# Kernel optimization log

Measured on AMD Instinct MI355X. Metric: run time of the kernel, lower is better.

The kernel has to match this reference:

```python
import jax, jax.numpy as jnp
import numpy as np

D_MODEL = 512
HEAD_NUM = 8
EPS = 1e-5


def setup_inputs() -> dict:
    key = jax.random.key(0)
    ks = jax.random.split(key, 7)
    B, S, D = 2, 4096, D_MODEL
    scale = 1.0 / np.sqrt(D)
    return {
        "x": jax.random.normal(ks[0], (B, S, D), dtype=jnp.float32),
        "Wq": jax.random.normal(ks[1], (D, D), dtype=jnp.float32) * scale,
        "bq": jnp.zeros((D,), dtype=jnp.float32),
        "Wk": jax.random.normal(ks[2], (D, D), dtype=jnp.float32) * scale,
        "bk": jnp.zeros((D,), dtype=jnp.float32),
        "Wv": jax.random.normal(ks[3], (D, D), dtype=jnp.float32) * scale,
        "bv": jnp.zeros((D,), dtype=jnp.float32),
        "gamma": jnp.ones((D,), dtype=jnp.float32),
        "beta": jnp.zeros((D,), dtype=jnp.float32),
    }


def reference(x, Wq, bq, Wk, bk, Wv, bv, gamma, beta):
    B, S, D = x.shape
    H = HEAD_NUM
    hd = D // H  # q_k_head_dim == v_head_dim == 64
    q = (x @ Wq + bq).reshape(B, H, S, hd)  # faithful to torch .view (no transpose)
    k = (x @ Wk + bk).reshape(B, H, S, hd)
    v = (x @ Wv + bv).reshape(B, H, S, hd)
    # [B,H,S,S] score matrix, materialized exactly as the original does
    scores = jnp.einsum("bhqd,bhkd->bhqk", q, k) / jnp.sqrt(jnp.float32(hd))
    attn_w = jax.nn.softmax(scores, axis=-1)
    attn = jnp.einsum("bhqk,bhkd->bhqd", attn_w, v).reshape(B, S, D)
    h = x + attn
    mu = jnp.mean(h, axis=-1, keepdims=True)
    var = jnp.var(h, axis=-1, keepdims=True)
    y = (h - mu) / jnp.sqrt(var + EPS) * gamma + beta
    return y
```

## Files before the change

### kernel.cpp

```cpp
#include <hip/hip_runtime.h>
#include <stdint.h>

#define D_ 512
#define S_ 4096
#define HD 64
#define CHUNK (S_*HD)

typedef short short8 __attribute__((ext_vector_type(8)));
typedef unsigned short ushort8 __attribute__((ext_vector_type(8)));
typedef float f32x16 __attribute__((ext_vector_type(16)));
typedef float f32x4 __attribute__((ext_vector_type(4)));

__device__ __forceinline__ float b2f(unsigned short u){
  unsigned x = ((unsigned)u) << 16;
  return __builtin_bit_cast(float, x);
}
__device__ __forceinline__ unsigned short f2b(float f){
  unsigned x = __builtin_bit_cast(unsigned, f);
  return (unsigned short)((x + 0x7fffu + ((x >> 16) & 1u)) >> 16);
}
__device__ __forceinline__ unsigned cvt_pk_bf16(float lo, float hi){
  unsigned r; asm("v_cvt_pk_bf16_f32 %0, %1, %2" : "=v"(r) : "v"(lo), "v"(hi)); return r;
}
__device__ __forceinline__ float fexp2(float x){
  float r; asm("v_exp_f32 %0, %1" : "=v"(r) : "v"(x)); return r;
}
__device__ __forceinline__ void gload16(const void* g, void* l){
  __builtin_amdgcn_global_load_lds((__attribute__((address_space(1))) void*)g,
                                   (__attribute__((address_space(3))) void*)l, 16, 0, 0);
}

__global__ void k_convert(const float* __restrict__ x, unsigned short* __restrict__ xb,
                          const float* __restrict__ Wq, const float* __restrict__ Wk,
                          const float* __restrict__ Wv, unsigned short* __restrict__ wt){
  __shared__ __align__(16) float t[32][33];
  if (blockIdx.x < 2048){
    int i = blockIdx.x * blockDim.x + threadIdx.x;
    const float4* xv = (const float4*)x;
    float4 a = xv[i*2], b = xv[i*2+1];
    ushort8 o;
    o[0]=f2b(a.x); o[1]=f2b(a.y); o[2]=f2b(a.z); o[3]=f2b(a.w);
    o[4]=f2b(b.x); o[5]=f2b(b.y); o[6]=f2b(b.z); o[7]=f2b(b.w);
    ((ushort8*)xb)[i] = o;
    return;
  }
  const int i = blockIdx.x - 2048;
  const int z = i >> 8, rem = i & 255;
  const int k0 = (rem & 15) * 32, n0 = (rem >> 4) * 32;
  const float* W = (z==0) ? Wq : ((z==1) ? Wk : Wv);
  unsigned short* o = wt + z * D_ * D_;
  int r = threadIdx.x >> 3, c4 = (threadIdx.x & 7) * 4;
  float4 vv = *(const float4*)&W[(k0+r)*D_ + n0 + c4];
  t[r][c4+0]=vv.x; t[r][c4+1]=vv.y; t[r][c4+2]=vv.z; t[r][c4+3]=vv.w;
  __syncthreads();
  unsigned short* dst = &o[(n0+r)*D_ + k0 + c4];
  dst[0]=f2b(t[c4+0][r]); dst[1]=f2b(t[c4+1][r]);
  dst[2]=f2b(t[c4+2][r]); dst[3]=f2b(t[c4+3][r]);
}

__global__ void __launch_bounds__(256) k_gemm(const unsigned short* __restrict__ xb,
                                              const unsigned short* __restrict__ wt,
                                              const float* __restrict__ bq,
                                              const float* __restrict__ bk,
                                              const float* __restrict__ bv,
                                              unsigned short* __restrict__ q,
                                              unsigned short* __restrict__ k,
                                              unsigned short* __restrict__ v){
  __shared__ __align__(16) unsigned short At[2][128*32];
  __shared__ __align__(16) unsigned short Bt[2][128*32];
  const int mat = blockIdx.z;
  const unsigned short* w = wt + mat * D_ * D_;
  const float* bias = (mat==0) ? bq : ((mat==1) ? bk : bv);
  unsigned short* out = (mat==0) ? q : ((mat==1) ? k : v);
  const int m0 = blockIdx.x * 128, n0 = blockIdx.y * 128;
  const int tid = threadIdx.x, lane = tid & 63, wv = tid >> 6;
  const int wm = wv >> 1, wn = wv & 1;
  const int l15 = lane & 15, l4 = lane >> 4;

  f32x4 acc[4][4] = {};

  auto stage = [&](int kt, int sel){
    const int kbase = kt * 32;
    #pragma unroll
    for (int j = 0; j < 2; j++){
      const int loff = wv*2048 + j*1024 + lane*16;
      const int row = loff >> 6;
      const int c = (loff >> 4) & 3;
      gload16(xb + (m0+row)*D_ + kbase + ((c ^ (row&3)) << 3),
              (char*)At[sel] + wv*2048 + j*1024);
      gload16(w  + (n0+row)*D_ + kbase + ((c ^ (row&3)) << 3),
              (char*)Bt[sel] + wv*2048 + j*1024);
    }
  };

  stage(0, 0);
  int buf = 0;
  for (int kt = 0; kt < 16; ++kt){
    __syncthreads();
    if (kt + 1 < 16) stage(kt + 1, buf ^ 1);
    short8 af[4], bf[4];
    #pragma unroll
    for (int mf = 0; mf < 4; mf++){
      const int row = wm*64 + mf*16 + l15;
      af[mf] = *(const short8*)((const char*)At[buf] + row*64 + ((l4*16) ^ ((row&3)<<4)));
    }
    #pragma unroll
    for (int nf = 0; nf < 4; nf++){
      const int row = wn*64 + nf*16 + l15;
      bf[nf] = *(const short8*)((const char*)Bt[buf] + row*64 + ((l4*16) ^ ((row&3)<<4)));
    }
    #pragma unroll
    for (int mf = 0; mf < 4; mf++)
      #pragma unroll
      for (int nf = 0; nf < 4; nf++)
        acc[mf][nf] = __builtin_amdgcn_mfma_f32_16x16x32_bf16(af[mf], bf[nf], acc[mf][nf], 0,0,0);
    buf ^= 1;
  }
  #pragma unroll
  for (int nf = 0; nf < 4; nf++){
    const int n = n0 + wn*64 + nf*16 + l15;
    const float bval = bias[n];
    #pragma unroll
    for (int mf = 0; mf < 4; mf++){
      #pragma unroll
      for (int r = 0; r < 4; r++){
        const int m = m0 + wm*64 + mf*16 + l4*4 + r;
        out[m*D_ + n] = f2b(acc[mf][nf][r] + bval);
      }
    }
  }
}

__global__ void k_transpose_v(const unsigned short* __restrict__ v, unsigned short* __restrict__ vt){
  __shared__ __align__(16) unsigned short t[64][72];
  const int bh = blockIdx.y, s0 = blockIdx.x * 64;
  const unsigned short* vc = v + bh * CHUNK;
  unsigned short* vtc = vt + bh * CHUNK;
  const int tid = threadIdx.x;
  #pragma unroll
  for (int j = 0; j < 2; j++){
    const int e = j*2048 + tid*8;
    const int row = e >> 6, col = e & 63;
    *(ushort8*)&t[row][col] = *(const ushort8*)&vc[(s0+row)*HD + col];
  }
  __syncthreads();
  const int d = tid >> 2, sc0 = (tid & 3) * 16;
  ushort8 o0, o1;
  #pragma unroll
  for (int j = 0; j < 4; j++){
    o0[j]   = t[sc0 + j     ][d];
    o0[j+4] = t[sc0 + 8 + j ][d];
    o1[j]   = t[sc0 + 4 + j ][d];
    o1[j+4] = t[sc0 + 12 + j][d];
  }
  *(ushort8*)&vtc[d*S_ + s0 + sc0]     = o0;
  *(ushort8*)&vtc[d*S_ + s0 + sc0 + 8] = o1;
}

__global__ void __launch_bounds__(256, 4) k_attn_part(const unsigned short* __restrict__ q,
                                                      const unsigned short* __restrict__ k,
                                                      const unsigned short* __restrict__ vt,
                                                      unsigned short* __restrict__ Op0,
                                                      unsigned short* __restrict__ Op1,
                                                      float2* __restrict__ ml0,
                                                      float2* __restrict__ ml1){
  __shared__ __align__(16) char smem[32768];
  const int bid = blockIdx.x;
  const int c8 = bid & 7, j = bid >> 3;
  const int bh   = 2*c8 + (j & 1);
  const int qblk = (j >> 1) & 31;
  const int half = (j >> 6) & 1;

  const int tid = threadIdx.x, lane = tid & 63, wv = tid >> 6;
  const int l31 = lane & 31, hi = lane >> 5;
  const unsigned short* qc  = q  + bh * CHUNK;
  const unsigned short* kc  = k  + bh * CHUNK;
  const unsigned short* vtc = vt + bh * CHUNK;
  unsigned short* Op = half ? Op1 : Op0;
  float2* ml = half ? ml1 : ml0;
  const int q0 = qblk * 128 + wv * 32;
  const int kvbase = half * 2048;

  short8 qf[4];
  {
    const int row = q0 + l31;
    #pragma unroll
    for (int kb = 0; kb < 4; kb++){
      ushort8 raw = *(const ushort8*)(qc + row*HD + kb*16 + hi*8);
      union { ushort8 u; short8 s; } cc;
      #pragma unroll
      for (int jj = 0; jj < 8; jj++) cc.u[jj] = f2b(b2f(raw[jj]) * (0.125f * 1.44269504f));
      qf[kb] = cc.s;
    }
  }

  f32x16 o0 = {}; f32x16 o1 = {};
  float lrun = 0.f;

  auto stage = [&](int t, int sel){
    const int kv0 = kvbase + t * 64;
    char* kb_ = smem + sel*8192 + wv*2048;
    char* vb_ = smem + 16384 + sel*8192 + wv*2048;
    #pragma unroll
    for (int jj = 0; jj < 2; jj++){
      const int loff = wv*2048 + jj*1024 + lane*16;
      const int row = loff >> 7;
      const int c = (loff >> 4) & 7;
      gload16(kc  + (kv0+row)*HD + ((c ^ (row&7)) << 3), kb_ + jj*1024);
      gload16(vtc + row*S_ + kv0 + ((c ^ (row&7)) << 3), vb_ + jj*1024);
    }
  };

  stage(0, 0);
  int buf = 0;
  const int NT = 2048 / 64;
  for (int t = 0; t < NT; ++t){
    __syncthreads();
    if (t + 1 < NT) stage(t + 1, buf ^ 1);
    const char* kbuf = smem + buf*8192;
    const char* vbuf = smem + 16384 + buf*8192;

    f32x16 st0 = {}; f32x16 st1 = {};
    const int xr = (l31 & 7) << 4;
    #pragma unroll
    for (int kb = 0; kb < 4; kb++){
      const int off = kb*32 + hi*16;
      short8 kf0 = *(const short8*)(kbuf + l31*128        + (off ^ xr));
      short8 kf1 = *(const short8*)(kbuf + (32+l31)*128   + (off ^ xr));
      st0 = __builtin_amdgcn_mfma_f32_32x32x16_bf16(kf0, qf[kb], st0, 0,0,0);
      st1 = __builtin_amdgcn_mfma_f32_32x32x16_bf16(kf1, qf[kb], st1, 0,0,0);
    }

    float s0a = 0.f, s1a = 0.f, s2a = 0.f, s3a = 0.f;
    #pragma unroll
    for (int r = 0; r < 8; r++){
      st0[r]   = fexp2(st0[r]);   s0a += st0[r];
      st0[r+8] = fexp2(st0[r+8]); s1a += st0[r+8];
      st1[r]   = fexp2(st1[r]);   s2a += st1[r];
      st1[r+8] = fexp2(st1[r+8]); s3a += st1[r+8];
    }
    float sum = (s0a + s1a) + (s2a + s3a);
    sum += __shfl_xor(sum, 32);
    lrun += sum;

    short8 pf[4];
    #pragma unroll
    for (int kb = 0; kb < 4; kb++){
      const f32x16& s = (kb < 2) ? st0 : st1;
      const int rb = (kb & 1) * 8;
      union { unsigned u[4]; short8 s8; } pu;
      pu.u[0] = cvt_pk_bf16(s[rb+0], s[rb+1]);
      pu.u[1] = cvt_pk_bf16(s[rb+2], s[rb+3]);
      pu.u[2] = cvt_pk_bf16(s[rb+4], s[rb+5]);
      pu.u[3] = cvt_pk_bf16(s[rb+6], s[rb+7]);
      pf[kb] = pu.s8;
    }

    #pragma unroll
    for (int kb = 0; kb < 4; kb++){
      const int off = kb*32 + hi*16;
      short8 vf0 = *(const short8*)(vbuf + l31*128      + (off ^ xr));
      short8 vf1 = *(const short8*)(vbuf + (32+l31)*128 + (off ^ xr));
      o0 = __builtin_amdgcn_mfma_f32_32x32x16_bf16(vf0, pf[kb], o0, 0,0,0);
      o1 = __builtin_amdgcn_mfma_f32_32x32x16_bf16(vf1, pf[kb], o1, 0,0,0);
    }
    buf ^= 1;
  }

  __syncthreads();
  {
    float* po = (float*)(void*)smem + wv*2048;
    #pragma unroll
    for (int r = 0; r < 16; r++){
      const int d = (r&3) + 8*(r>>2) + 4*hi;
      po[l31*64 + d]      = o0[r];
      po[l31*64 + 32 + d] = o1[r];
    }
  }
  if (hi == 0){
    ml[bh*S_ + q0 + l31] = make_float2(0.0f, lrun);
  }
  __syncthreads();
  {
    const int rr = lane >> 1, hf = lane & 1;
    const float* prow = (const float*)(void*)smem + wv*2048 + rr*64 + hf*32;
    unsigned short* dst = Op + (bh*S_ + q0 + rr)*HD + hf*32;
    #pragma unroll
    for (int blk = 0; blk < 4; blk++){
      ushort8 w8;
      #pragma unroll
      for (int jj = 0; jj < 8; jj++) w8[jj] = f2b(prow[blk*8 + jj]);
      *(ushort8*)(dst + blk*8) = w8;
    }
  }
}

__global__ void k_merge_ln(const unsigned short* __restrict__ Op0,
                           const unsigned short* __restrict__ Op1,
                           const float2* __restrict__ ml0,
                           const float2* __restrict__ ml1,
                           const float* __restrict__ x,
                           const float* __restrict__ gamma,
                           const float* __restrict__ beta,
                           float* __restrict__ out){
  const int row = blockIdx.x * 4 + (threadIdx.x >> 6);
  const int lane = threadIdx.x & 63;
  const int bh = row >> 9;
  const int s_attn = ((row & 511) << 3) + (lane >> 3);
  const int d0 = (lane & 7) * 8;
  const int oidx = (bh*S_ + s_attn)*HD + d0;
  ushort8 u0 = *(const ushort8*)(Op0 + oidx);
  ushort8 u1 = *(const ushort8*)(Op1 + oidx);
  const float2 a = ml0[bh*S_ + s_attn];
  const float2 c = ml1[bh*S_ + s_attn];
  const float M  = fmaxf(a.x, c.x);
  const float e1 = exp2f(a.x - M), e2 = exp2f(c.x - M);
  const float inv = 1.0f / (e1*a.y + e2*c.y);
  const float w1 = e1 * inv, w2 = e2 * inv;

  const float* xr = x + row*D_ + lane*8;
  float4 a0 = *(const float4*)xr, a1 = *(const float4*)(xr + 4);
  float h[8];
  h[0]=a0.x; h[1]=a0.y; h[2]=a0.z; h[3]=a0.w; h[4]=a1.x; h[5]=a1.y; h[6]=a1.z; h[7]=a1.w;
  #pragma unroll
  for (int jj = 0; jj < 8; jj++) h[jj] += w1*b2f(u0[jj]) + w2*b2f(u1[jj]);

  float sm = 0.f, ss = 0.f;
  #pragma unroll
  for (int jj = 0; jj < 8; jj++){ sm += h[jj]; ss += h[jj]*h[jj]; }
  #pragma unroll
  for (int msk = 1; msk < 64; msk <<= 1){ sm += __shfl_xor(sm, msk); ss += __shfl_xor(ss, msk); }
  const float mu = sm * (1.f/512.f);
  const float var = ss * (1.f/512.f) - mu*mu;
  const float rs = rsqrtf(var + 1e-5f);
  const float* g = gamma + lane*8;
  const float* be = beta + lane*8;
  float4 w0, w3;
  w0.x = (h[0]-mu)*rs*g[0] + be[0];
  w0.y = (h[1]-mu)*rs*g[1] + be[1];
  w0.z = (h[2]-mu)*rs*g[2] + be[2];
  w0.w = (h[3]-mu)*rs*g[3] + be[3];
  w3.x = (h[4]-mu)*rs*g[4] + be[4];
  w3.y = (h[5]-mu)*rs*g[5] + be[5];
  w3.z = (h[6]-mu)*rs*g[6] + be[6];
  w3.w = (h[7]-mu)*rs*g[7] + be[7];
  float* op = out + row*D_ + lane*8;
  *(float4*)op = w0;
  *(float4*)(op + 4) = w3;
}

extern "C" void kernel_launch(void* const* d_in, const int* in_sizes, int n_in,
                              void* d_out, int out_size, void* d_ws, size_t ws_size,
                              hipStream_t stream){
  const float* x     = (const float*)d_in[0];
  const float* Wq    = (const float*)d_in[1];
  const float* bq    = (const float*)d_in[2];
  const float* Wk    = (const float*)d_in[3];
  const float* bk    = (const float*)d_in[4];
  const float* Wv    = (const float*)d_in[5];
  const float* bv    = (const float*)d_in[6];
  const float* gamma = (const float*)d_in[7];
  const float* beta  = (const float*)d_in[8];
  float* out = (float*)d_out;

  char* ws = (char*)d_ws;
  unsigned short* wt = (unsigned short*)(ws);
  unsigned short* q  = (unsigned short*)(ws + 1572864);
  unsigned short* k  = (unsigned short*)(ws + 9961472);
  unsigned short* v  = (unsigned short*)(ws + 18350080);
  unsigned short* vt = (unsigned short*)(ws + 26738688);
  unsigned short* Op0 = v;
  unsigned short* Op1 = (unsigned short*)(ws + 35127296);
  float2* ml0 = (float2*)(ws + 43515904);
  float2* ml1 = (float2*)(ws + 44040192);
  unsigned short* xb = (unsigned short*)((char*)d_out + 8388608);

  k_convert    <<<2816, 256, 0, stream>>>(x, xb, Wq, Wk, Wv, wt);
  k_gemm       <<<dim3(64,4,3),  256, 0, stream>>>(xb, wt, bq, bk, bv, q, k, v);
  k_transpose_v<<<dim3(64,16),   256, 0, stream>>>(v, vt);
  k_attn_part  <<<1024, 256, 0, stream>>>(q, k, vt, Op0, Op1, ml0, ml1);
  k_merge_ln   <<<2048, 256, 0, stream>>>(Op0, Op1, ml0, ml1, x, gamma, beta, out);
}
```

Measured before the change: 122.4 us.

## Fuse V transpose into GEMM epilogue and keep attention partials in fp32

Removes the separate V transpose kernel: the projection GEMM now writes V straight into the transposed, lane-permuted layout the attention kernel expects. Attention partial outputs are stored as fp32 instead of bf16, and one partial buffer is aliased onto the output tensor, which the merge/layernorm kernel reads and overwrites in place. This saves a kernel launch, the V round trip and the bf16 pack/unpack. The costs are strided 2-byte scatter stores in the GEMM epilogue and doubled traffic for the partial outputs.

```diff
diff --git a/kernel.cpp b/kernel.cpp
--- a/kernel.cpp
+++ b/kernel.cpp
@@ -65,13 +65,13 @@
                                               const float* __restrict__ bv,
                                               unsigned short* __restrict__ q,
                                               unsigned short* __restrict__ k,
-                                              unsigned short* __restrict__ v){
+                                              unsigned short* __restrict__ vt){
   __shared__ __align__(16) unsigned short At[2][128*32];
   __shared__ __align__(16) unsigned short Bt[2][128*32];
   const int mat = blockIdx.z;
   const unsigned short* w = wt + mat * D_ * D_;
   const float* bias = (mat==0) ? bq : ((mat==1) ? bk : bv);
-  unsigned short* out = (mat==0) ? q : ((mat==1) ? k : v);
+  unsigned short* out = (mat==0) ? q : ((mat==1) ? k : vt);
   const int m0 = blockIdx.x * 128, n0 = blockIdx.y * 128;
   const int tid = threadIdx.x, lane = tid & 63, wv = tid >> 6;
   const int wm = wv >> 1, wn = wv & 1;
@@ -116,52 +116,47 @@
         acc[mf][nf] = __builtin_amdgcn_mfma_f32_16x16x32_bf16(af[mf], bf[nf], acc[mf][nf], 0,0,0);
     buf ^= 1;
   }
-  #pragma unroll
-  for (int nf = 0; nf < 4; nf++){
-    const int n = n0 + wn*64 + nf*16 + l15;
-    const float bval = bias[n];
-    #pragma unroll
-    for (int mf = 0; mf < 4; mf++){
+  if (mat == 2){
+    #pragma unroll
+    for (int nf = 0; nf < 4; nf++){
+      const int n = n0 + wn*64 + nf*16 + l15;
+      const float bval = bias[n];
+      const int d = n & 63, nh = n >> 6;
       #pragma unroll
-      for (int r = 0; r < 4; r++){
-        const int m = m0 + wm*64 + mf*16 + l4*4 + r;
-        out[m*D_ + n] = f2b(acc[mf][nf][r] + bval);
+      for (int mf = 0; mf < 4; mf++){
+        #pragma unroll
+        for (int r = 0; r < 4; r++){
+          const int m = m0 + wm*64 + mf*16 + l4*4 + r;
+          const int bh = m >> 9;
+          const int sl = ((m & 511) << 3) + nh;
+          const int s4 = sl & 15;
+          const int sp = (sl & ~15) | (s4 & 3) | ((s4 & 4) << 1) | ((s4 & 8) >> 1);
+          out[bh*CHUNK + d*S_ + sp] = f2b(acc[mf][nf][r] + bval);
+        }
       }
     }
-  }
-}
-
-__global__ void k_transpose_v(const unsigned short* __restrict__ v, unsigned short* __restrict__ vt){
-  __shared__ __align__(16) unsigned short t[64][72];
-  const int bh = blockIdx.y, s0 = blockIdx.x * 64;
-  const unsigned short* vc = v + bh * CHUNK;
-  unsigned short* vtc = vt + bh * CHUNK;
-  const int tid = threadIdx.x;
-  #pragma unroll
-  for (int j = 0; j < 2; j++){
-    const int e = j*2048 + tid*8;
-    const int row = e >> 6, col = e & 63;
-    *(ushort8*)&t[row][col] = *(const ushort8*)&vc[(s0+row)*HD + col];
-  }
-  __syncthreads();
-  const int d = tid >> 2, sc0 = (tid & 3) * 16;
-  ushort8 o0, o1;
-  #pragma unroll
-  for (int j = 0; j < 4; j++){
-    o0[j]   = t[sc0 + j     ][d];
-    o0[j+4] = t[sc0 + 8 + j ][d];
-    o1[j]   = t[sc0 + 4 + j ][d];
-    o1[j+4] = t[sc0 + 12 + j][d];
-  }
-  *(ushort8*)&vtc[d*S_ + s0 + sc0]     = o0;
-  *(ushort8*)&vtc[d*S_ + s0 + sc0 + 8] = o1;
+  } else {
+    #pragma unroll
+    for (int nf = 0; nf < 4; nf++){
+      const int n = n0 + wn*64 + nf*16 + l15;
+      const float bval = bias[n];
+      #pragma unroll
+      for (int mf = 0; mf < 4; mf++){
+        #pragma unroll
+        for (int r = 0; r < 4; r++){
+          const int m = m0 + wm*64 + mf*16 + l4*4 + r;
+          out[m*D_ + n] = f2b(acc[mf][nf][r] + bval);
+        }
+      }
+    }
+  }
 }
 
 __global__ void __launch_bounds__(256, 4) k_attn_part(const unsigned short* __restrict__ q,
                                                       const unsigned short* __restrict__ k,
                                                       const unsigned short* __restrict__ vt,
-                                                      unsigned short* __restrict__ Op0,
-                                                      unsigned short* __restrict__ Op1,
+                                                      float* __restrict__ Op0,
+                                                      float* __restrict__ Op1,
                                                       float2* __restrict__ ml0,
                                                       float2* __restrict__ ml1){
   __shared__ __align__(16) char smem[32768];
@@ -176,7 +171,7 @@
   const unsigned short* qc  = q  + bh * CHUNK;
   const unsigned short* kc  = k  + bh * CHUNK;
   const unsigned short* vtc = vt + bh * CHUNK;
-  unsigned short* Op = half ? Op1 : Op0;
+  float* Op = half ? Op1 : Op0;
   float2* ml = half ? ml1 : ml0;
   const int q0 = qblk * 128 + wv * 32;
   const int kvbase = half * 2048;
@@ -284,33 +279,32 @@
   {
     const int rr = lane >> 1, hf = lane & 1;
     const float* prow = (const float*)(void*)smem + wv*2048 + rr*64 + hf*32;
-    unsigned short* dst = Op + (bh*S_ + q0 + rr)*HD + hf*32;
-    #pragma unroll
-    for (int blk = 0; blk < 4; blk++){
-      ushort8 w8;
-      #pragma unroll
-      for (int jj = 0; jj < 8; jj++) w8[jj] = f2b(prow[blk*8 + jj]);
-      *(ushort8*)(dst + blk*8) = w8;
-    }
-  }
-}
-
-__global__ void k_merge_ln(const unsigned short* __restrict__ Op0,
-                           const unsigned short* __restrict__ Op1,
+    float* dst = Op + (bh*S_ + q0 + rr)*HD + hf*32;
+    #pragma unroll
+    for (int blk = 0; blk < 8; blk++){
+      *(float4*)(dst + blk*4) = *(const float4*)(prow + blk*4);
+    }
+  }
+}
+
+__global__ void k_merge_ln(const float* Op0,
+                           const float* Op1,
                            const float2* __restrict__ ml0,
                            const float2* __restrict__ ml1,
                            const float* __restrict__ x,
                            const float* __restrict__ gamma,
                            const float* __restrict__ beta,
-                           float* __restrict__ out){
+                           float* out){
   const int row = blockIdx.x * 4 + (threadIdx.x >> 6);
   const int lane = threadIdx.x & 63;
   const int bh = row >> 9;
   const int s_attn = ((row & 511) << 3) + (lane >> 3);
   const int d0 = (lane & 7) * 8;
   const int oidx = (bh*S_ + s_attn)*HD + d0;
-  ushort8 u0 = *(const ushort8*)(Op0 + oidx);
-  ushort8 u1 = *(const ushort8*)(Op1 + oidx);
+  float4 f0a = *(const float4*)(Op0 + oidx);
+  float4 f0b = *(const float4*)(Op0 + oidx + 4);
+  float4 f1a = *(const float4*)(Op1 + oidx);
+  float4 f1b = *(const float4*)(Op1 + oidx + 4);
   const float2 a = ml0[bh*S_ + s_attn];
   const float2 c = ml1[bh*S_ + s_attn];
   const float M  = fmaxf(a.x, c.x);
@@ -321,9 +315,14 @@
   const float* xr = x + row*D_ + lane*8;
   float4 a0 = *(const float4*)xr, a1 = *(const float4*)(xr + 4);
   float h[8];
-  h[0]=a0.x; h[1]=a0.y; h[2]=a0.z; h[3]=a0.w; h[4]=a1.x; h[5]=a1.y; h[6]=a1.z; h[7]=a1.w;
-  #pragma unroll
-  for (int jj = 0; jj < 8; jj++) h[jj] += w1*b2f(u0[jj]) + w2*b2f(u1[jj]);
+  h[0]=a0.x + w1*f0a.x + w2*f1a.x;
+  h[1]=a0.y + w1*f0a.y + w2*f1a.y;
+  h[2]=a0.z + w1*f0a.z + w2*f1a.z;
+  h[3]=a0.w + w1*f0a.w + w2*f1a.w;
+  h[4]=a1.x + w1*f0b.x + w2*f1b.x;
+  h[5]=a1.y + w1*f0b.y + w2*f1b.y;
+  h[6]=a1.z + w1*f0b.z + w2*f1b.z;
+  h[7]=a1.w + w1*f0b.w + w2*f1b.w;
 
   float sm = 0.f, ss = 0.f;
   #pragma unroll
@@ -367,17 +366,15 @@
   unsigned short* wt = (unsigned short*)(ws);
   unsigned short* q  = (unsigned short*)(ws + 1572864);
   unsigned short* k  = (unsigned short*)(ws + 9961472);
-  unsigned short* v  = (unsigned short*)(ws + 18350080);
-  unsigned short* vt = (unsigned short*)(ws + 26738688);
-  unsigned short* Op0 = v;
-  unsigned short* Op1 = (unsigned short*)(ws + 35127296);
+  unsigned short* vt = (unsigned short*)(ws + 18350080);
+  float* Op1 = (float*)(ws + 26738688);
   float2* ml0 = (float2*)(ws + 43515904);
   float2* ml1 = (float2*)(ws + 44040192);
+  float* Op0 = out;
   unsigned short* xb = (unsigned short*)((char*)d_out + 8388608);
 
-  k_convert    <<<2816, 256, 0, stream>>>(x, xb, Wq, Wk, Wv, wt);
-  k_gemm       <<<dim3(64,4,3),  256, 0, stream>>>(xb, wt, bq, bk, bv, q, k, v);
-  k_transpose_v<<<dim3(64,16),   256, 0, stream>>>(v, vt);
-  k_attn_part  <<<1024, 256, 0, stream>>>(q, k, vt, Op0, Op1, ml0, ml1);
-  k_merge_ln   <<<2048, 256, 0, stream>>>(Op0, Op1, ml0, ml1, x, gamma, beta, out);
-}
+  k_convert   <<<2816, 256, 0, stream>>>(x, xb, Wq, Wk, Wv, wt);
+  k_gemm      <<<dim3(64,4,3),  256, 0, stream>>>(xb, wt, bq, bk, bv, q, k, vt);
+  k_attn_part <<<1024, 256, 0, stream>>>(q, k, vt, Op0, Op1, ml0, ml1);
+  k_merge_ln  <<<2048, 256, 0, stream>>>(Op0, Op1, ml0, ml1, x, gamma, beta, out);
+}
```

Result: slower. 156.8 us (+28.2%).
